# Kernel tuning notes

Hardware: AMD Instinct MI355X
Metric: run time of the kernel (lower is better)

## Reference

```python
import jax, jax.numpy as jnp
import numpy as np

HEADS = 4


def setup_inputs() -> dict:
    key = jax.random.key(0)
    kx, kqkv, kbq, ko, kbo = jax.random.split(key, 5)
    B, C, H, W = 4, 256, 64, 64
    x = jax.random.normal(kx, (B, C, H, W), dtype=jnp.float32)
    # torch nn.Linear stores weight as [out_features, in_features]
    w_qkv = jax.random.normal(kqkv, (3 * C, C), dtype=jnp.float32) * (1.0 / np.sqrt(C))
    b_qkv = jax.random.normal(kbq, (3 * C,), dtype=jnp.float32) * 0.02
    w_o = jax.random.normal(ko, (C, C), dtype=jnp.float32) * (1.0 / np.sqrt(C))
    b_o = jax.random.normal(kbo, (C,), dtype=jnp.float32) * 0.02
    return {"x": x, "w_qkv": w_qkv, "b_qkv": b_qkv, "w_o": w_o, "b_o": b_o}


def reference(x, w_qkv, b_qkv, w_o, b_o):
    B, C, H, W = x.shape
    S = H * W
    hd = C // HEADS
    # (B, C, H, W) -> (B, S, C)
    xt = x.reshape(B, C, S).transpose(0, 2, 1)
    qkv = xt @ w_qkv.T + b_qkv                      # (B, S, 3C)
    q, k, v = jnp.split(qkv, 3, axis=-1)
    def to_heads(t):
        return t.reshape(B, S, HEADS, hd).transpose(0, 2, 1, 3)  # (B, h, S, hd)
    q, k, v = to_heads(q), to_heads(k), to_heads(v)
    scores = jnp.einsum('bhqd,bhkd->bhqk', q, k) / jnp.sqrt(jnp.float32(hd))
    attn = jax.nn.softmax(scores, axis=-1)          # dropout inactive (eval)
    out = jnp.einsum('bhqk,bhkd->bhqd', attn, v)    # (B, h, S, hd)
    out = out.transpose(0, 2, 1, 3).reshape(B, S, C)
    y = out @ w_o.T + b_o                            # (B, S, C)
    y = y.reshape(B, H, W, C).transpose(0, 3, 1, 2)  # (B, C, H, W)
    return y
```

## Files before the change

### kernel.cpp

```cpp
#include <hip/hip_runtime.h>
#include <stdint.h>

#define DI __device__ __forceinline__

typedef __attribute__((ext_vector_type(8))) __bf16 bf16x8;
typedef __attribute__((ext_vector_type(8))) unsigned short u16x8;
typedef __attribute__((ext_vector_type(4))) float f32x4;
typedef __attribute__((ext_vector_type(4))) uint32_t u32x4;
typedef unsigned short u16;

constexpr int Bb = 4, Cc = 256, Ss = 4096, HD = 64;
constexpr int ELEMS = Bb * Cc * Ss;

DI float bf2f(u16 h) { union { unsigned u; float f; } x; x.u = ((unsigned)h) << 16; return x.f; }
DI u16 f2bf(float f) {
  union { float f; unsigned u; } x; x.f = f;
  return (u16)((x.u + 0x7FFFu + ((x.u >> 16) & 1u)) >> 16);
}
DI uint32_t pack2bf_trunc(float a, float b) {
  union { float f; uint32_t u; } xa, xb;
  xa.f = a; xb.f = b;
  return __builtin_amdgcn_perm(xb.u, xa.u, 0x07060302u);
}
DI bf16x8 ldfrag(const u16* p) { return __builtin_bit_cast(bf16x8, *(const u16x8*)p); }

DI void g2l16(const u16* g, u16* l) {
  __builtin_amdgcn_global_load_lds((const __attribute__((address_space(1))) uint32_t*)(const void*)g,
                                   (__attribute__((address_space(3))) uint32_t*)(void*)l, 16, 0, 0);
}

__global__ __launch_bounds__(256) void k_transpose(const float* __restrict__ x, u16* __restrict__ xt,
                                                   const float* __restrict__ wq, const float* __restrict__ wo,
                                                   u16* __restrict__ wqb, u16* __restrict__ wob) {
  __shared__ u16 T[64][72];
  const int st = blockIdx.x, ct = blockIdx.y, b = blockIdx.z;
  const int tid = threadIdx.x;
  {
    int flat = blockIdx.x + 64 * blockIdx.y + 256 * blockIdx.z;
    int widx = flat * 256 + tid;
    if (widx < 196608) wqb[widx] = f2bf(wq[widx]);
    else wob[widx - 196608] = f2bf(wo[widx - 196608]);
  }
#pragma unroll
  for (int e = 0; e < 2; e++) {
    int ss = tid + e * 256;
    int r = ss >> 3, seg = ss & 7;
    size_t base = ((size_t)(b * Cc + ct * 64 + r) << 12) + st * 64 + seg * 8;
    u16x8 t;
#pragma unroll
    for (int j = 0; j < 8; j++) t[j] = f2bf(x[base + j]);
    *(u16x8*)&T[r][(seg ^ ((r >> 3) & 7)) * 8] = t;
  }
  __syncthreads();
#pragma unroll
  for (int e = 0; e < 2; e++) {
    int ss = tid + e * 256;
    int sr = ss >> 3, cseg = ss & 7;
    u16x8 o;
#pragma unroll
    for (int j = 0; j < 8; j++) {
      int row = cseg * 8 + j;
      o[j] = T[row][(((sr >> 3) ^ cseg) * 8) + (sr & 7)];
    }
    *(u16x8*)(xt + ((size_t)(b * Ss + st * 64 + sr) << 8) + ct * 64 + cseg * 8) = o;
  }
}

DI void stage_tile(const u16* __restrict__ src, int pitch, int r0, int k0, u16 (*dst)[40], int tid) {
#pragma unroll
  for (int e = 0; e < 2; e++) {
    int c = tid + e * 256;
    int row = c >> 2, seg = c & 3;
    u16x8 t = *(const u16x8*)(src + (size_t)(r0 + row) * pitch + k0 + seg * 8);
    *(u16x8*)&dst[row][seg * 8] = t;
  }
}

__global__ __launch_bounds__(256) void k_qkv(const u16* __restrict__ xt, const u16* __restrict__ w,
                                             const float* __restrict__ bias,
                                             u16* __restrict__ q, u16* __restrict__ kk_, u16* __restrict__ vv_) {
  __shared__ u16 As[128][40], Bs[128][40];
  const int tid = threadIdx.x;
  const int wv = tid >> 6, lane = tid & 63;
  const int wm = wv >> 1, wn = wv & 1;
  const int lr = lane & 15, quad = lane >> 4;
  const int r0 = blockIdx.x * 128;
  const int j0 = blockIdx.y * 128;
  f32x4 acc[4][4] = {};
  for (int k0 = 0; k0 < 256; k0 += 32) {
    __syncthreads();
    stage_tile(xt, 256, r0, k0, As, tid);
    stage_tile(w, 256, j0, k0, Bs, tid);
    __syncthreads();
    bf16x8 a[4], b[4];
#pragma unroll
    for (int mt = 0; mt < 4; mt++) a[mt] = ldfrag(&As[wm * 64 + mt * 16 + lr][quad * 8]);
#pragma unroll
    for (int nt = 0; nt < 4; nt++) b[nt] = ldfrag(&Bs[wn * 64 + nt * 16 + lr][quad * 8]);
#pragma unroll
    for (int mt = 0; mt < 4; mt++)
#pragma unroll
      for (int nt = 0; nt < 4; nt++)
        acc[mt][nt] = __builtin_amdgcn_mfma_f32_16x16x32_bf16(a[mt], b[nt], acc[mt][nt], 0, 0, 0);
  }
#pragma unroll
  for (int nt = 0; nt < 4; nt++) {
    int j = j0 + wn * 64 + nt * 16 + lr;
    float bj = bias[j];
    int part = j >> 8, cc = j & 255, head = cc >> 6, d = cc & 63;
    u16* outp = (part == 0) ? q : (part == 1) ? kk_ : vv_;
    float sc = (part == 0) ? 0.18033688f : 1.0f;
#pragma unroll
    for (int mt = 0; mt < 4; mt++)
#pragma unroll
      for (int rg = 0; rg < 4; rg++) {
        int row = r0 + wm * 64 + mt * 16 + quad * 4 + rg;
        int b_ = row >> 12, s = row & 4095;
        outp[((size_t)((b_ * 4 + head) * Ss + s) << 6) + d] = f2bf((acc[mt][nt][rg] + bj) * sc);
      }
  }
}

__global__ __launch_bounds__(256) void k_vt(const u16* __restrict__ v, u16* __restrict__ vt) {
  __shared__ u16 T[64][72];
  const int chunk = blockIdx.x, bh = blockIdx.y;
  const int tid = threadIdx.x;
#pragma unroll
  for (int e = 0; e < 2; e++) {
    int row = (tid >> 3) + e * 32, seg = tid & 7;
    *(u16x8*)&T[row][(seg ^ ((row >> 3) & 7)) * 8] =
        *(const u16x8*)(v + ((size_t)(bh * Ss + chunk * 64 + row) << 6) + seg * 8);
  }
  __syncthreads();
#pragma unroll
  for (int e = 0; e < 2; e++) {
    int d = (tid >> 3) + e * 32, seg = tid & 7;
    u16x8 o;
#pragma unroll
    for (int j = 0; j < 8; j++) {
      int slot = seg * 8 + j;
      int t = (((slot >> 5) & 1) << 1) | ((slot >> 2) & 1);
      int w6 = t * 16 + (((slot >> 3) & 3) << 2) + (slot & 3);
      o[j] = T[w6][(((d >> 3) ^ ((w6 >> 3) & 7)) * 8) + (d & 7)];
    }
    *(u16x8*)(vt + ((size_t)(bh * 64 + d) << 12) + chunk * 64 + seg * 8) = o;
  }
}

__global__ __launch_bounds__(256, 3) void k_attn(const u16* __restrict__ Q, const u16* __restrict__ K,
                                                 const u16* __restrict__ VT, u16* __restrict__ AO,
                                                 u16* __restrict__ AOP, float* __restrict__ lpart,
                                                 int nsplit) {
  __shared__ u16 Kl[2][64][64];
  __shared__ u16 Vl[2][64][64];
  const int tid = threadIdx.x;
  const int wv = tid >> 6, lane = tid & 63;
  const int lr = lane & 15, quad = lane >> 4;
  const int bh = blockIdx.y;
  const int b_ = bh >> 2, head = bh & 3;
  const int qbase = blockIdx.x * 256 + wv * 64;
  const int sp = blockIdx.z;
  const int nchunk = 64 / nsplit, kcg0 = sp * nchunk;
  const u16* Qh = Q + (size_t)bh * Ss * HD;
  const u16* Kh = K + (size_t)bh * Ss * HD;
  const u16* Vh = VT + (size_t)bh * HD * Ss;

  bf16x8 qb[4][2];
#pragma unroll
  for (int nt = 0; nt < 4; nt++)
#pragma unroll
    for (int ks = 0; ks < 2; ks++)
      qb[nt][ks] = ldfrag(Qh + (size_t)(qbase + nt * 16 + lr) * HD + ks * 32 + quad * 8);

  u16x8 ov;
#pragma unroll
  for (int j = 0; j < 8; j++) ov[j] = 0x3F80;
  const bf16x8 ones = __builtin_bit_cast(bf16x8, ov);

  f32x4 O[4][4] = {};
  f32x4 lacc[4] = {};

  const int lrow = lane >> 3;
  const int lseg = ((lane & 7) ^ lrow) * 8;
  const int kd0 = wv * 16 + lrow;
  const u16* pK0 = Kh + ((size_t)(kcg0 * 64 + kd0) << 6) + lseg;
  const u16* pK1 = pK0 + (8 << 6);
  const u16* pV0 = Vh + ((size_t)kd0 << 12) + kcg0 * 64 + lseg;
  const u16* pV1 = pV0 + ((size_t)8 << 12);
  auto stage = [&](int buf) {
    g2l16(pK0, &Kl[buf][wv * 16][0]);
    g2l16(pK1, &Kl[buf][wv * 16 + 8][0]);
    g2l16(pV0, &Vl[buf][wv * 16][0]);
    g2l16(pV1, &Vl[buf][wv * 16 + 8][0]);
    pK0 += 4096; pK1 += 4096; pV0 += 64; pV1 += 64;
  };

  stage(0);
  __syncthreads();

  for (int kc = 0; kc < nchunk; kc++) {
    const int cur = kc & 1;
    if (kc + 1 < nchunk) stage(cur ^ 1);

#pragma unroll
    for (int h = 0; h < 2; h++) {
      uint32_t pk[2][4][2];
#pragma unroll
      for (int kt2 = 0; kt2 < 2; kt2++) {
        const int krow = (h * 2 + kt2) * 16 + lr;
        bf16x8 ka0 = ldfrag(&Kl[cur][krow][(quad ^ (lr & 7)) * 8]);
        bf16x8 ka1 = ldfrag(&Kl[cur][krow][((4 + quad) ^ (lr & 7)) * 8]);
        f32x4 St[4] = {};
        __builtin_amdgcn_s_setprio(1);
#pragma unroll
        for (int nt = 0; nt < 4; nt++)
          St[nt] = __builtin_amdgcn_mfma_f32_16x16x32_bf16(ka0, qb[nt][0], St[nt], 0, 0, 0);
#pragma unroll
        for (int nt = 0; nt < 4; nt++)
          St[nt] = __builtin_amdgcn_mfma_f32_16x16x32_bf16(ka1, qb[nt][1], St[nt], 0, 0, 0);
        __builtin_amdgcn_s_setprio(0);
#pragma unroll
        for (int nt = 0; nt < 4; nt++) {
          float p0 = __builtin_amdgcn_exp2f(St[nt][0]);
          float p1 = __builtin_amdgcn_exp2f(St[nt][1]);
          float p2 = __builtin_amdgcn_exp2f(St[nt][2]);
          float p3 = __builtin_amdgcn_exp2f(St[nt][3]);
          pk[kt2][nt][0] = pack2bf_trunc(p0, p1);
          pk[kt2][nt][1] = pack2bf_trunc(p2, p3);
        }
      }
      bf16x8 pa[4];
#pragma unroll
      for (int mt = 0; mt < 4; mt++) {
        u32x4 t = {pk[0][mt][0], pk[0][mt][1], pk[1][mt][0], pk[1][mt][1]};
        pa[mt] = __builtin_bit_cast(bf16x8, t);
      }
#pragma unroll
      for (int dt = 0; dt < 4; dt++) {
        bf16x8 vb = ldfrag(&Vl[cur][dt * 16 + lr][((h * 4 + quad) ^ (lr & 7)) * 8]);
        __builtin_amdgcn_s_setprio(1);
#pragma unroll
        for (int mt = 0; mt < 4; mt++)
          O[mt][dt] = __builtin_amdgcn_mfma_f32_16x16x32_bf16(pa[mt], vb, O[mt][dt], 0, 0, 0);
        __builtin_amdgcn_s_setprio(0);
      }
#pragma unroll
      for (int mt = 0; mt < 4; mt++)
        lacc[mt] = __builtin_amdgcn_mfma_f32_16x16x32_bf16(pa[mt], ones, lacc[mt], 0, 0, 0);
    }

    __syncthreads();
  }

  u16* dst = (nsplit == 1) ? AO : (AOP + (size_t)sp * ELEMS);
  if (nsplit > 1 && lr == 0) {
    float* lp = lpart + (size_t)sp * (16 * Ss) + bh * Ss;
#pragma unroll
    for (int mt = 0; mt < 4; mt++)
#pragma unroll
      for (int rg = 0; rg < 4; rg++) lp[qbase + mt * 16 + quad * 4 + rg] = lacc[mt][rg];
  }
#pragma unroll
  for (int mt = 0; mt < 4; mt++)
#pragma unroll
    for (int rg = 0; rg < 4; rg++) {
      float inv = 1.0f / lacc[mt][rg];
      int s = qbase + mt * 16 + quad * 4 + rg;
#pragma unroll
      for (int dt = 0; dt < 4; dt++)
        dst[((size_t)(b_ * Ss + s) << 8) + head * 64 + dt * 16 + lr] = f2bf(O[mt][dt][rg] * inv);
    }
}

__global__ __launch_bounds__(256) void k_oproj(const u16* __restrict__ wo, const u16* __restrict__ ao,
                                               const u16* __restrict__ AOP, const float* __restrict__ lpart,
                                               const float* __restrict__ bo, float* __restrict__ y, int nsplit) {
  __shared__ u16 As[128][40], Bs[128][40];
  const int tid = threadIdx.x;
  const int wv = tid >> 6, lane = tid & 63;
  const int wm = wv >> 1, wn = wv & 1;
  const int lr = lane & 15, quad = lane >> 4;
  const int n0 = blockIdx.x * 128;
  const int m0 = blockIdx.y * 128;
  f32x4 acc[4][4] = {};
  for (int k0 = 0; k0 < 256; k0 += 32) {
    __syncthreads();
    stage_tile(wo, 256, m0, k0, As, tid);
#pragma unroll
    for (int e = 0; e < 2; e++) {
      int c = tid + e * 256;
      int row = c >> 2, seg = c & 3;
      int bs = n0 + row, cc = k0 + seg * 8;
      u16x8 t;
      if (nsplit == 1) {
        t = *(const u16x8*)(ao + ((size_t)bs << 8) + cc);
      } else {
        int b = bs >> 12, s = bs & 4095, head = cc >> 6;
        int li = (b * 4 + head) * Ss + s;
        float accv[8] = {0.f, 0.f, 0.f, 0.f, 0.f, 0.f, 0.f, 0.f};
        float lsum = 0.f;
        for (int spl = 0; spl < nsplit; spl++) {
          float l = lpart[(size_t)spl * (16 * Ss) + li];
          u16x8 a = *(const u16x8*)(AOP + (size_t)spl * ELEMS + ((size_t)bs << 8) + cc);
          lsum += l;
#pragma unroll
          for (int i = 0; i < 8; i++) accv[i] += l * bf2f(a[i]);
        }
        float inv = 1.0f / lsum;
#pragma unroll
        for (int i = 0; i < 8; i++) t[i] = f2bf(accv[i] * inv);
      }
      *(u16x8*)&Bs[row][seg * 8] = t;
    }
    __syncthreads();
    bf16x8 a[4], b[4];
#pragma unroll
    for (int mt = 0; mt < 4; mt++) a[mt] = ldfrag(&As[wm * 64 + mt * 16 + lr][quad * 8]);
#pragma unroll
    for (int nt = 0; nt < 4; nt++) b[nt] = ldfrag(&Bs[wn * 64 + nt * 16 + lr][quad * 8]);
#pragma unroll
    for (int mt = 0; mt < 4; mt++)
#pragma unroll
      for (int nt = 0; nt < 4; nt++)
        acc[mt][nt] = __builtin_amdgcn_mfma_f32_16x16x32_bf16(a[mt], b[nt], acc[mt][nt], 0, 0, 0);
  }
#pragma unroll
  for (int mt = 0; mt < 4; mt++)
#pragma unroll
    for (int rg = 0; rg < 4; rg++) {
      int c = m0 + wm * 64 + mt * 16 + quad * 4 + rg;
      float bc = bo[c];
#pragma unroll
      for (int nt = 0; nt < 4; nt++) {
        int col = n0 + wn * 64 + nt * 16 + lr;
        int b_ = col >> 12, s = col & 4095;
        y[((size_t)(b_ * Cc + c) << 12) + s] = acc[mt][nt][rg] + bc;
      }
    }
}

extern "C" void kernel_launch(void* const* d_in, const int* in_sizes, int n_in,
                              void* d_out, int out_size, void* d_ws, size_t ws_size,
                              hipStream_t stream) {
  const float* x = (const float*)d_in[0];
  const float* w_qkv = (const float*)d_in[1];
  const float* b_qkv = (const float*)d_in[2];
  const float* w_o = (const float*)d_in[3];
  const float* b_o = (const float*)d_in[4];
  float* y = (float*)d_out;
  u16* ws = (u16*)d_ws;
  u16* xt = ws;
  u16* q = ws + (size_t)ELEMS;
  u16* k = ws + (size_t)2 * ELEMS;
  u16* vt = ws + (size_t)3 * ELEMS;
  u16* ao = xt;
  u16* wqb = ws + (size_t)4 * ELEMS;
  u16* wob = wqb + 196608;
  const size_t Wu16 = (size_t)4 * ELEMS + 262144;
  auto need = [&](int n) { return (Wu16 + (size_t)n * ELEMS) * 2 + (size_t)n * 16 * Ss * 4; };
  const int nsplit = (ws_size >= need(4)) ? 4 : (ws_size >= need(2)) ? 2 : 1;
  u16* aop = ws + Wu16;
  u16* v = aop;
  float* lpart = (float*)(aop + (size_t)nsplit * ELEMS);

  k_transpose<<<dim3(64, 4, 4), 256, 0, stream>>>(x, xt, w_qkv, w_o, wqb, wob);
  k_qkv<<<dim3(128, 6), 256, 0, stream>>>(xt, wqb, b_qkv, q, k, v);
  k_vt<<<dim3(64, 16), 256, 0, stream>>>(v, vt);
  k_attn<<<dim3(16, 16, nsplit), 256, 0, stream>>>(q, k, vt, ao, aop, lpart, nsplit);
  k_oproj<<<dim3(128, 2), 256, 0, stream>>>(wob, ao, aop, lpart, b_o, y, nsplit);
}
```

Baseline: 188.8 us.

## Software-pipeline attention so QK of chunk k overlaps PV of chunk k-1

Restructures the attention main loop so the QK^T MFMAs and exp of the current key chunk are interleaved with the PV MFMAs of the previous chunk. P fragments ping-pong between two register sets, and V gets a triple-buffered LDS slot so the previous chunk's V stays valid while the next one is staged. To fit the extra registers, the launch bound drops from 3 to 2 blocks per SM and the split-K factor drops from 4 to 2. The goal is to hide exp and VALU latency behind matrix work, at the cost of lower occupancy and fewer, longer blocks.

```diff
diff --git a/kernel.cpp b/kernel.cpp
--- a/kernel.cpp
+++ b/kernel.cpp
@@ -1,5 +1,6 @@
 #include <hip/hip_runtime.h>
 #include <stdint.h>
+#include <type_traits>
 
 #define DI __device__ __forceinline__
 
@@ -147,12 +148,12 @@
   }
 }
 
-__global__ __launch_bounds__(256, 3) void k_attn(const u16* __restrict__ Q, const u16* __restrict__ K,
+__global__ __launch_bounds__(256, 2) void k_attn(const u16* __restrict__ Q, const u16* __restrict__ K,
                                                  const u16* __restrict__ VT, u16* __restrict__ AO,
                                                  u16* __restrict__ AOP, float* __restrict__ lpart,
                                                  int nsplit) {
   __shared__ u16 Kl[2][64][64];
-  __shared__ u16 Vl[2][64][64];
+  __shared__ u16 Vl[3][64][64];
   const int tid = threadIdx.x;
   const int wv = tid >> 6, lane = tid & 63;
   const int lr = lane & 15, quad = lane >> 4;
@@ -187,69 +188,86 @@
   const u16* pK1 = pK0 + (8 << 6);
   const u16* pV0 = Vh + ((size_t)kd0 << 12) + kcg0 * 64 + lseg;
   const u16* pV1 = pV0 + ((size_t)8 << 12);
-  auto stage = [&](int buf) {
-    g2l16(pK0, &Kl[buf][wv * 16][0]);
-    g2l16(pK1, &Kl[buf][wv * 16 + 8][0]);
-    g2l16(pV0, &Vl[buf][wv * 16][0]);
-    g2l16(pV1, &Vl[buf][wv * 16 + 8][0]);
+  auto stage = [&](int kb, int vbuf) {
+    g2l16(pK0, &Kl[kb][wv * 16][0]);
+    g2l16(pK1, &Kl[kb][wv * 16 + 8][0]);
+    g2l16(pV0, &Vl[vbuf][wv * 16][0]);
+    g2l16(pV1, &Vl[vbuf][wv * 16 + 8][0]);
     pK0 += 4096; pK1 += 4096; pV0 += 64; pV1 += 64;
   };
 
-  stage(0);
+  u32x4 paA[2][4], paB[2][4];
+
+  auto pv_slice = [&](int t, u32x4 (&paR)[2][4], int vprev) {
+    const int hp = t >> 1, dt0 = (t & 1) * 2;
+#pragma unroll
+    for (int dd = 0; dd < 2; dd++) {
+      const int dt = dt0 + dd;
+      bf16x8 vb = ldfrag(&Vl[vprev][dt * 16 + lr][((hp * 4 + quad) ^ (lr & 7)) * 8]);
+      __builtin_amdgcn_s_setprio(1);
+#pragma unroll
+      for (int mt = 0; mt < 4; mt++)
+        O[mt][dt] = __builtin_amdgcn_mfma_f32_16x16x32_bf16(
+            __builtin_bit_cast(bf16x8, paR[hp][mt]), vb, O[mt][dt], 0, 0, 0);
+      __builtin_amdgcn_s_setprio(0);
+    }
+    if (t & 1) {
+#pragma unroll
+      for (int mt = 0; mt < 4; mt++)
+        lacc[mt] = __builtin_amdgcn_mfma_f32_16x16x32_bf16(
+            __builtin_bit_cast(bf16x8, paR[hp][mt]), ones, lacc[mt], 0, 0, 0);
+    }
+  };
+
+  auto body = [&](int kc, auto dopv, auto dostage, u32x4 (&paW)[2][4], u32x4 (&paR)[2][4]) {
+    const int cur = kc & 1;
+    const int vprev = (kc + 2) % 3;
+    if constexpr (decltype(dostage)::value) stage((kc + 1) & 1, (kc + 1) % 3);
+#pragma unroll
+    for (int t = 0; t < 4; t++) {
+      const int krow = t * 16 + lr;
+      bf16x8 ka0 = ldfrag(&Kl[cur][krow][(quad ^ (lr & 7)) * 8]);
+      bf16x8 ka1 = ldfrag(&Kl[cur][krow][((4 + quad) ^ (lr & 7)) * 8]);
+      f32x4 St[4] = {};
+      __builtin_amdgcn_s_setprio(1);
+#pragma unroll
+      for (int nt = 0; nt < 4; nt++)
+        St[nt] = __builtin_amdgcn_mfma_f32_16x16x32_bf16(ka0, qb[nt][0], St[nt], 0, 0, 0);
+#pragma unroll
+      for (int nt = 0; nt < 4; nt++)
+        St[nt] = __builtin_amdgcn_mfma_f32_16x16x32_bf16(ka1, qb[nt][1], St[nt], 0, 0, 0);
+      __builtin_amdgcn_s_setprio(0);
+      if constexpr (decltype(dopv)::value) pv_slice(t, paR, vprev);
+      const int h = t >> 1, k2 = (t & 1) * 2;
+#pragma unroll
+      for (int nt = 0; nt < 4; nt++) {
+        float p0 = __builtin_amdgcn_exp2f(St[nt][0]);
+        float p1 = __builtin_amdgcn_exp2f(St[nt][1]);
+        float p2 = __builtin_amdgcn_exp2f(St[nt][2]);
+        float p3 = __builtin_amdgcn_exp2f(St[nt][3]);
+        paW[h][nt][k2] = pack2bf_trunc(p0, p1);
+        paW[h][nt][k2 + 1] = pack2bf_trunc(p2, p3);
+      }
+    }
+    __syncthreads();
+  };
+
+  using TT = std::bool_constant<true>;
+  using FF = std::bool_constant<false>;
+
+  stage(0, 0);
   __syncthreads();
-
-  for (int kc = 0; kc < nchunk; kc++) {
-    const int cur = kc & 1;
-    if (kc + 1 < nchunk) stage(cur ^ 1);
-
-#pragma unroll
-    for (int h = 0; h < 2; h++) {
-      uint32_t pk[2][4][2];
-#pragma unroll
-      for (int kt2 = 0; kt2 < 2; kt2++) {
-        const int krow = (h * 2 + kt2) * 16 + lr;
-        bf16x8 ka0 = ldfrag(&Kl[cur][krow][(quad ^ (lr & 7)) * 8]);
-        bf16x8 ka1 = ldfrag(&Kl[cur][krow][((4 + quad) ^ (lr & 7)) * 8]);
-        f32x4 St[4] = {};
-        __builtin_amdgcn_s_setprio(1);
-#pragma unroll
-        for (int nt = 0; nt < 4; nt++)
-          St[nt] = __builtin_amdgcn_mfma_f32_16x16x32_bf16(ka0, qb[nt][0], St[nt], 0, 0, 0);
-#pragma unroll
-        for (int nt = 0; nt < 4; nt++)
-          St[nt] = __builtin_amdgcn_mfma_f32_16x16x32_bf16(ka1, qb[nt][1], St[nt], 0, 0, 0);
-        __builtin_amdgcn_s_setprio(0);
-#pragma unroll
-        for (int nt = 0; nt < 4; nt++) {
-          float p0 = __builtin_amdgcn_exp2f(St[nt][0]);
-          float p1 = __builtin_amdgcn_exp2f(St[nt][1]);
-          float p2 = __builtin_amdgcn_exp2f(St[nt][2]);
-          float p3 = __builtin_amdgcn_exp2f(St[nt][3]);
-          pk[kt2][nt][0] = pack2bf_trunc(p0, p1);
-          pk[kt2][nt][1] = pack2bf_trunc(p2, p3);
-        }
-      }
-      bf16x8 pa[4];
-#pragma unroll
-      for (int mt = 0; mt < 4; mt++) {
-        u32x4 t = {pk[0][mt][0], pk[0][mt][1], pk[1][mt][0], pk[1][mt][1]};
-        pa[mt] = __builtin_bit_cast(bf16x8, t);
-      }
-#pragma unroll
-      for (int dt = 0; dt < 4; dt++) {
-        bf16x8 vb = ldfrag(&Vl[cur][dt * 16 + lr][((h * 4 + quad) ^ (lr & 7)) * 8]);
-        __builtin_amdgcn_s_setprio(1);
-#pragma unroll
-        for (int mt = 0; mt < 4; mt++)
-          O[mt][dt] = __builtin_amdgcn_mfma_f32_16x16x32_bf16(pa[mt], vb, O[mt][dt], 0, 0, 0);
-        __builtin_amdgcn_s_setprio(0);
-      }
-#pragma unroll
-      for (int mt = 0; mt < 4; mt++)
-        lacc[mt] = __builtin_amdgcn_mfma_f32_16x16x32_bf16(pa[mt], ones, lacc[mt], 0, 0, 0);
-    }
-
-    __syncthreads();
+  body(0, FF{}, TT{}, paA, paB);
+  int kc = 1;
+  for (; kc + 2 < nchunk; kc += 2) {
+    body(kc, TT{}, TT{}, paB, paA);
+    body(kc + 1, TT{}, TT{}, paA, paB);
+  }
+  body(nchunk - 1, TT{}, FF{}, paB, paA);
+  {
+    const int vlast = (nchunk - 1) % 3;
+#pragma unroll
+    for (int t = 0; t < 4; t++) pv_slice(t, paB, vlast);
   }
 
   u16* dst = (nsplit == 1) ? AO : (AOP + (size_t)sp * ELEMS);
@@ -358,7 +376,7 @@
   u16* wob = wqb + 196608;
   const size_t Wu16 = (size_t)4 * ELEMS + 262144;
   auto need = [&](int n) { return (Wu16 + (size_t)n * ELEMS) * 2 + (size_t)n * 16 * Ss * 4; };
-  const int nsplit = (ws_size >= need(4)) ? 4 : (ws_size >= need(2)) ? 2 : 1;
+  const int nsplit = (ws_size >= need(2)) ? 2 : 1;
   u16* aop = ws + Wu16;
   u16* v = aop;
   float* lpart = (float*)(aop + (size_t)nsplit * ELEMS);
```

New measurement: 179.5 us. 5.0% less time.

## Halve attention query tile per wave, sum softmax denominator on VALU, use 2-way split

Applied to the files above, without the earlier changes.

Each wave now handles 32 queries instead of 64, and the attention grid doubles along the query axis. The split over the key dimension drops from 4 to 2, which keeps the block count the same while halving the partial outputs the output projection must merge. The row sum of exp values moves from an extra MFMA against a ones vector to VALU adds of bf16-truncated values followed by cross-lane shuffles. This lowers register pressure and removes MFMA work, but each K/V chunk loaded into LDS is now reused by fewer queries, so more K/V traffic per query.

```diff
diff --git a/kernel.cpp b/kernel.cpp
--- a/kernel.cpp
+++ b/kernel.cpp
@@ -21,6 +21,9 @@
   union { float f; uint32_t u; } xa, xb;
   xa.f = a; xb.f = b;
   return __builtin_amdgcn_perm(xb.u, xa.u, 0x07060302u);
+}
+DI float truncbf(float f) {
+  union { float f; unsigned u; } x; x.f = f; x.u &= 0xFFFF0000u; return x.f;
 }
 DI bf16x8 ldfrag(const u16* p) { return __builtin_bit_cast(bf16x8, *(const u16x8*)p); }
 
@@ -158,27 +161,22 @@
   const int lr = lane & 15, quad = lane >> 4;
   const int bh = blockIdx.y;
   const int b_ = bh >> 2, head = bh & 3;
-  const int qbase = blockIdx.x * 256 + wv * 64;
+  const int qbase = blockIdx.x * 128 + wv * 32;
   const int sp = blockIdx.z;
   const int nchunk = 64 / nsplit, kcg0 = sp * nchunk;
   const u16* Qh = Q + (size_t)bh * Ss * HD;
   const u16* Kh = K + (size_t)bh * Ss * HD;
   const u16* Vh = VT + (size_t)bh * HD * Ss;
 
-  bf16x8 qb[4][2];
-#pragma unroll
-  for (int nt = 0; nt < 4; nt++)
+  bf16x8 qb[2][2];
+#pragma unroll
+  for (int nt = 0; nt < 2; nt++)
 #pragma unroll
     for (int ks = 0; ks < 2; ks++)
       qb[nt][ks] = ldfrag(Qh + (size_t)(qbase + nt * 16 + lr) * HD + ks * 32 + quad * 8);
 
-  u16x8 ov;
-#pragma unroll
-  for (int j = 0; j < 8; j++) ov[j] = 0x3F80;
-  const bf16x8 ones = __builtin_bit_cast(bf16x8, ov);
-
-  f32x4 O[4][4] = {};
-  f32x4 lacc[4] = {};
+  f32x4 O[2][4] = {};
+  float lsum[2] = {0.f, 0.f};
 
   const int lrow = lane >> 3;
   const int lseg = ((lane & 7) ^ lrow) * 8;
@@ -202,69 +200,75 @@
     const int cur = kc & 1;
     if (kc + 1 < nchunk) stage(cur ^ 1);
 
-#pragma unroll
-    for (int h = 0; h < 2; h++) {
-      uint32_t pk[2][4][2];
-#pragma unroll
-      for (int kt2 = 0; kt2 < 2; kt2++) {
-        const int krow = (h * 2 + kt2) * 16 + lr;
-        bf16x8 ka0 = ldfrag(&Kl[cur][krow][(quad ^ (lr & 7)) * 8]);
-        bf16x8 ka1 = ldfrag(&Kl[cur][krow][((4 + quad) ^ (lr & 7)) * 8]);
-        f32x4 St[4] = {};
-        __builtin_amdgcn_s_setprio(1);
-#pragma unroll
-        for (int nt = 0; nt < 4; nt++)
-          St[nt] = __builtin_amdgcn_mfma_f32_16x16x32_bf16(ka0, qb[nt][0], St[nt], 0, 0, 0);
-#pragma unroll
-        for (int nt = 0; nt < 4; nt++)
-          St[nt] = __builtin_amdgcn_mfma_f32_16x16x32_bf16(ka1, qb[nt][1], St[nt], 0, 0, 0);
-        __builtin_amdgcn_s_setprio(0);
-#pragma unroll
-        for (int nt = 0; nt < 4; nt++) {
-          float p0 = __builtin_amdgcn_exp2f(St[nt][0]);
-          float p1 = __builtin_amdgcn_exp2f(St[nt][1]);
-          float p2 = __builtin_amdgcn_exp2f(St[nt][2]);
-          float p3 = __builtin_amdgcn_exp2f(St[nt][3]);
-          pk[kt2][nt][0] = pack2bf_trunc(p0, p1);
-          pk[kt2][nt][1] = pack2bf_trunc(p2, p3);
-        }
-      }
-      bf16x8 pa[4];
-#pragma unroll
-      for (int mt = 0; mt < 4; mt++) {
-        u32x4 t = {pk[0][mt][0], pk[0][mt][1], pk[1][mt][0], pk[1][mt][1]};
-        pa[mt] = __builtin_bit_cast(bf16x8, t);
-      }
+    u32x4 pa[2][2];
+#pragma unroll
+    for (int t = 0; t < 4; t++) {
+      const int krow = t * 16 + lr;
+      bf16x8 ka0 = ldfrag(&Kl[cur][krow][(quad ^ (lr & 7)) * 8]);
+      bf16x8 ka1 = ldfrag(&Kl[cur][krow][((4 + quad) ^ (lr & 7)) * 8]);
+      f32x4 St[2] = {};
+      __builtin_amdgcn_s_setprio(1);
+#pragma unroll
+      for (int nt = 0; nt < 2; nt++)
+        St[nt] = __builtin_amdgcn_mfma_f32_16x16x32_bf16(ka0, qb[nt][0], St[nt], 0, 0, 0);
+#pragma unroll
+      for (int nt = 0; nt < 2; nt++)
+        St[nt] = __builtin_amdgcn_mfma_f32_16x16x32_bf16(ka1, qb[nt][1], St[nt], 0, 0, 0);
+      __builtin_amdgcn_s_setprio(0);
+      const int h = t >> 1, k2 = (t & 1) * 2;
+#pragma unroll
+      for (int nt = 0; nt < 2; nt++) {
+        float p0 = __builtin_amdgcn_exp2f(St[nt][0]);
+        float p1 = __builtin_amdgcn_exp2f(St[nt][1]);
+        float p2 = __builtin_amdgcn_exp2f(St[nt][2]);
+        float p3 = __builtin_amdgcn_exp2f(St[nt][3]);
+        pa[h][nt][k2] = pack2bf_trunc(p0, p1);
+        pa[h][nt][k2 + 1] = pack2bf_trunc(p2, p3);
+        lsum[nt] += (truncbf(p0) + truncbf(p1)) + (truncbf(p2) + truncbf(p3));
+      }
+    }
+#pragma unroll
+    for (int h = 0; h < 2; h++)
 #pragma unroll
       for (int dt = 0; dt < 4; dt++) {
         bf16x8 vb = ldfrag(&Vl[cur][dt * 16 + lr][((h * 4 + quad) ^ (lr & 7)) * 8]);
         __builtin_amdgcn_s_setprio(1);
 #pragma unroll
-        for (int mt = 0; mt < 4; mt++)
-          O[mt][dt] = __builtin_amdgcn_mfma_f32_16x16x32_bf16(pa[mt], vb, O[mt][dt], 0, 0, 0);
+        for (int mt = 0; mt < 2; mt++)
+          O[mt][dt] = __builtin_amdgcn_mfma_f32_16x16x32_bf16(
+              __builtin_bit_cast(bf16x8, pa[h][mt]), vb, O[mt][dt], 0, 0, 0);
         __builtin_amdgcn_s_setprio(0);
       }
-#pragma unroll
-      for (int mt = 0; mt < 4; mt++)
-        lacc[mt] = __builtin_amdgcn_mfma_f32_16x16x32_bf16(pa[mt], ones, lacc[mt], 0, 0, 0);
-    }
-
-    __syncthreads();
-  }
+    __syncthreads();
+  }
+
+  float lfull[2];
+#pragma unroll
+  for (int nt = 0; nt < 2; nt++) {
+    float r = lsum[nt] + __shfl_xor(lsum[nt], 16, 64);
+    r += __shfl_xor(r, 32, 64);
+    lfull[nt] = r;
+  }
+  float lval[2][4];
+#pragma unroll
+  for (int mt = 0; mt < 2; mt++)
+#pragma unroll
+    for (int rg = 0; rg < 4; rg++)
+      lval[mt][rg] = __shfl(lfull[mt], quad * 4 + rg, 64);
 
   u16* dst = (nsplit == 1) ? AO : (AOP + (size_t)sp * ELEMS);
   if (nsplit > 1 && lr == 0) {
     float* lp = lpart + (size_t)sp * (16 * Ss) + bh * Ss;
 #pragma unroll
-    for (int mt = 0; mt < 4; mt++)
-#pragma unroll
-      for (int rg = 0; rg < 4; rg++) lp[qbase + mt * 16 + quad * 4 + rg] = lacc[mt][rg];
-  }
-#pragma unroll
-  for (int mt = 0; mt < 4; mt++)
+    for (int mt = 0; mt < 2; mt++)
+#pragma unroll
+      for (int rg = 0; rg < 4; rg++) lp[qbase + mt * 16 + quad * 4 + rg] = lval[mt][rg];
+  }
+#pragma unroll
+  for (int mt = 0; mt < 2; mt++)
 #pragma unroll
     for (int rg = 0; rg < 4; rg++) {
-      float inv = 1.0f / lacc[mt][rg];
+      float inv = 1.0f / lval[mt][rg];
       int s = qbase + mt * 16 + quad * 4 + rg;
 #pragma unroll
       for (int dt = 0; dt < 4; dt++)
@@ -358,7 +362,7 @@
   u16* wob = wqb + 196608;
   const size_t Wu16 = (size_t)4 * ELEMS + 262144;
   auto need = [&](int n) { return (Wu16 + (size_t)n * ELEMS) * 2 + (size_t)n * 16 * Ss * 4; };
-  const int nsplit = (ws_size >= need(4)) ? 4 : (ws_size >= need(2)) ? 2 : 1;
+  const int nsplit = (ws_size >= need(2)) ? 2 : 1;
   u16* aop = ws + Wu16;
   u16* v = aop;
   float* lpart = (float*)(aop + (size_t)nsplit * ELEMS);
@@ -366,6 +370,6 @@
   k_transpose<<<dim3(64, 4, 4), 256, 0, stream>>>(x, xt, w_qkv, w_o, wqb, wob);
   k_qkv<<<dim3(128, 6), 256, 0, stream>>>(xt, wqb, b_qkv, q, k, v);
   k_vt<<<dim3(64, 16), 256, 0, stream>>>(v, vt);
-  k_attn<<<dim3(16, 16, nsplit), 256, 0, stream>>>(q, k, vt, ao, aop, lpart, nsplit);
+  k_attn<<<dim3(32, 16, nsplit), 256, 0, stream>>>(q, k, vt, ao, aop, lpart, nsplit);
   k_oproj<<<dim3(128, 2), 256, 0, stream>>>(wob, ao, aop, lpart, b_o, y, nsplit);
 }
```

New measurement: 193.6 us. 1.03x slower.
